# Performance work log

Hardware: AMD Instinct MI355X
Metric: run time of the kernel (lower is better)

Reference implementation:

```python
import jax, jax.numpy as jnp
import numpy as np

IN_F, OUT_F, RANK = 4096, 4096, 64
ALPHA = 128.0
SCALING = ALPHA / RANK  # 2.0
BATCH_TOKENS = 8192


def setup_inputs() -> dict:
    key = jax.random.key(0)
    k1, k2, k3, k4 = jax.random.split(key, 4)
    x = jax.random.normal(k1, (BATCH_TOKENS, IN_F), dtype=jnp.float32)
    weight = jax.random.normal(k2, (OUT_F, IN_F), dtype=jnp.float32) * 0.02
    P = jax.random.normal(k3, (OUT_F, RANK), dtype=jnp.float32) * 0.01
    Lambda = jnp.ones((RANK,), dtype=jnp.float32) * 0.01
    Q = jax.random.normal(k4, (RANK, IN_F), dtype=jnp.float32) * 0.01
    rank_mask = jnp.ones((RANK,), dtype=jnp.bool_)
    return {"x": x, "weight": weight, "P": P, "Lambda": Lambda, "Q": Q, "rank_mask": rank_mask}


def reference(x, weight, P, Lambda, Q, rank_mask):
    # active_Lambda = Lambda * mask; delta_W = (P * active_Lambda) @ Q  -> [OUT_F, IN_F]
    active_Lambda = Lambda * rank_mask.astype(Lambda.dtype)
    delta_W = (P * active_Lambda[None, :]) @ Q
    # F.linear(x, W_eff) = x @ W_eff^T
    W_eff = weight + SCALING * delta_W
    return x @ W_eff.T
```

## Files before the change

kernel.cpp:

```cpp
#include <hip/hip_runtime.h>
#include <hip/hip_bf16.h>
#include <stdint.h>

#define M_TOK 8192
#define NF    4096
#define KF    4096
#define RANK  64

typedef __attribute__((ext_vector_type(8))) short short8;
typedef __attribute__((ext_vector_type(4))) float floatx4;

typedef const uint32_t __attribute__((address_space(1)))* gp1_t;
typedef uint32_t __attribute__((address_space(3)))* lp3_t;

__device__ __forceinline__ void load_lds16(const void* g, void* l) {
  __builtin_amdgcn_global_load_lds((gp1_t)g, (lp3_t)l, 16, 0, 0);
}

__global__ void cast_f32_bf16(const float* __restrict__ in,
                              __hip_bfloat16* __restrict__ out) {
  size_t i = ((size_t)blockIdx.x * blockDim.x + threadIdx.x) * 8;
  float4 a = *(const float4*)(in + i);
  float4 b = *(const float4*)(in + i + 4);
  union { __hip_bfloat16 h[8]; uint4 u; } pk;
  pk.h[0] = __float2bfloat16(a.x);
  pk.h[1] = __float2bfloat16(a.y);
  pk.h[2] = __float2bfloat16(a.z);
  pk.h[3] = __float2bfloat16(a.w);
  pk.h[4] = __float2bfloat16(b.x);
  pk.h[5] = __float2bfloat16(b.y);
  pk.h[6] = __float2bfloat16(b.z);
  pk.h[7] = __float2bfloat16(b.w);
  *(uint4*)(out + i) = pk.u;
}

__global__ __launch_bounds__(256) void build_weff(
    const float* __restrict__ W, const float* __restrict__ P,
    const float* __restrict__ Lam, const float* __restrict__ Q,
    const unsigned char* __restrict__ mask,
    __hip_bfloat16* __restrict__ Wb) {
  __shared__ float lam[RANK];
  __shared__ float plT[RANK][68];
  __shared__ float Qs[RANK][68];

  const int t = threadIdx.x;
  const int n0 = blockIdx.y * 64;
  const int k0 = blockIdx.x * 64;

  if (t < RANK) lam[t] = 2.0f * Lam[t] * (mask[t] ? 1.0f : 0.0f);
  __syncthreads();

  {
    const int nl = t & 63;
    const int rg = (t >> 6) * 16;
    const float* p = P + (size_t)(n0 + nl) * RANK + rg;
#pragma unroll
    for (int j = 0; j < 16; j += 4) {
      float4 v = *(const float4*)(p + j);
      plT[rg + j + 0][nl] = v.x * lam[rg + j + 0];
      plT[rg + j + 1][nl] = v.y * lam[rg + j + 1];
      plT[rg + j + 2][nl] = v.z * lam[rg + j + 2];
      plT[rg + j + 3][nl] = v.w * lam[rg + j + 3];
    }
    const int r = t >> 2;
    const int kc = (t & 3) * 16;
    const float* q = Q + (size_t)r * KF + k0 + kc;
#pragma unroll
    for (int j = 0; j < 16; j += 4) {
      float4 v = *(const float4*)(q + j);
      Qs[r][kc + j + 0] = v.x;
      Qs[r][kc + j + 1] = v.y;
      Qs[r][kc + j + 2] = v.z;
      Qs[r][kc + j + 3] = v.w;
    }
  }
  __syncthreads();

  const int tn4 = t >> 4;
  const int tk4 = t & 15;
  float accv[4][4];
#pragma unroll
  for (int i = 0; i < 4; i++) {
    float4 w = *(const float4*)(W + (size_t)(n0 + tn4 * 4 + i) * KF + k0 + tk4 * 4);
    accv[i][0] = w.x; accv[i][1] = w.y; accv[i][2] = w.z; accv[i][3] = w.w;
  }
#pragma unroll 8
  for (int r = 0; r < RANK; r++) {
    float4 p4 = *(const float4*)&plT[r][tn4 * 4];
    float4 q4 = *(const float4*)&Qs[r][tk4 * 4];
#define ROWFMA(i, pi)                                                  \
    accv[i][0] += (pi) * q4.x; accv[i][1] += (pi) * q4.y;              \
    accv[i][2] += (pi) * q4.z; accv[i][3] += (pi) * q4.w;
    ROWFMA(0, p4.x) ROWFMA(1, p4.y) ROWFMA(2, p4.z) ROWFMA(3, p4.w)
#undef ROWFMA
  }
#pragma unroll
  for (int i = 0; i < 4; i++) {
    union { __hip_bfloat16 h[4]; uint2 u; } pk;
    pk.h[0] = __float2bfloat16(accv[i][0]);
    pk.h[1] = __float2bfloat16(accv[i][1]);
    pk.h[2] = __float2bfloat16(accv[i][2]);
    pk.h[3] = __float2bfloat16(accv[i][3]);
    *(uint2*)(Wb + (size_t)(n0 + tn4 * 4 + i) * KF + k0 + tk4 * 4) = pk.u;
  }
}

#define BM 256
#define BN 256
#define BK 64
#define NT (KF / BK)
#define ASL 16384

#define SB0 __builtin_amdgcn_sched_barrier(0)
#define BARSYNC do { SB0; __builtin_amdgcn_s_barrier(); } while (0)
#define LGK(n) do { asm volatile("s_waitcnt lgkmcnt(" #n ")" ::: "memory"); SB0; } while (0)

__device__ __forceinline__ void read_a4(short8 (&afr)[2][2],
                                        const __hip_bfloat16* Asl,
                                        int row_base, int swz) {
#pragma unroll
  for (int mm = 0; mm < 2; ++mm)
#pragma unroll
    for (int ks = 0; ks < 2; ++ks)
      afr[mm][ks] = *(const short8*)(Asl + ks * 8192 + (row_base + mm * 16) * 32 + swz);
}

__device__ __forceinline__ void read_b8(short8 (&bfr)[4][2],
                                        const __hip_bfloat16* Bsl,
                                        int brow, int swz) {
#pragma unroll
  for (int nf = 0; nf < 4; ++nf)
#pragma unroll
    for (int ks = 0; ks < 2; ++ks)
      bfr[nf][ks] = *(const short8*)(Bsl + ks * 8192 + (brow + nf * 16) * 32 + swz);
}

template <int P>
__device__ __forceinline__ void mfma16(floatx4 (&acc)[8][4],
                                       const short8 (&afr)[2][2],
                                       const short8 (&bfr)[4][2]) {
#pragma unroll
  for (int ks = 0; ks < 2; ++ks)
#pragma unroll
    for (int mm = 0; mm < 2; ++mm)
#pragma unroll
      for (int nf = 0; nf < 4; ++nf)
        acc[P * 2 + mm][nf] = __builtin_amdgcn_mfma_f32_16x16x32_bf16(
            afr[mm][ks], bfr[nf][ks], acc[P * 2 + mm][nf], 0, 0, 0);
}

__global__ __launch_bounds__(512, 2) void gemm_xwt(
    const __hip_bfloat16* __restrict__ A,
    const __hip_bfloat16* __restrict__ B,
    float* __restrict__ C) {
  extern __shared__ __hip_bfloat16 lds[];
  __hip_bfloat16* As = lds;
  __hip_bfloat16* Bs = lds + 2 * ASL;
  const __hip_bfloat16* As0 = As;
  const __hip_bfloat16* As1 = As + ASL;
  const __hip_bfloat16* Bs0 = Bs;
  const __hip_bfloat16* Bs1 = Bs + ASL;

  const int t = threadIdx.x;
  const int lane = t & 63;
  const int wave = t >> 6;
  const int wm = wave >> 2;
  const int wn = wave & 3;
  const int frow = lane & 15;
  const int kq = lane >> 4;
  const int swz = ((kq + (frow >> 1)) & 3) * 8;

  const int bid = blockIdx.x;
  const int wk = (bid & 7) * 64 + (bid >> 3);
  const int bm = wk >> 4;
  const int bn = wk & 15;

  const int c = ((t & 3) - ((t >> 3) & 3)) & 3;
  const __hip_bfloat16* a_src = A + (size_t)(bm * BM + (t >> 2)) * KF + c * 8;
  const __hip_bfloat16* b_src = B + (size_t)(bn * BN + (t >> 2)) * KF + c * 8;
  __hip_bfloat16* a_dst = As + t * 8;
  __hip_bfloat16* b_dst = Bs + t * 8;

#define STAGE_A(kt_, slot_, h_)                                                        \
  do {                                                                                 \
    const __hip_bfloat16* s_ = a_src + ((kt_) & (NT - 1)) * BK + (size_t)(h_) * 128 * KF; \
    __hip_bfloat16* d_ = a_dst + (slot_) * ASL + (h_) * 4096;                          \
    load_lds16(s_, d_);                                                \
    load_lds16(s_ + 32, d_ + 8192);                                    \
  } while (0)
#define STAGE_B(kt_, slot_, h_)                                                        \
  do {                                                                                 \
    const __hip_bfloat16* s_ = b_src + ((kt_) & (NT - 1)) * BK + (size_t)(h_) * 128 * KF; \
    __hip_bfloat16* d_ = b_dst + (slot_) * ASL + (h_) * 4096;                          \
    load_lds16(s_, d_);                                                                \
    load_lds16(s_ + 32, d_ + 8192);                                                    \
  } while (0)

  floatx4 acc[8][4] = {};
  short8 bE[4][2], bO[4][2];
  short8 aX[2][2], aY[2][2];

  const int arow = wm * 128 + frow;
  const int brow = wn * 64 + frow;

  STAGE_A(0, 0, 0); STAGE_A(0, 0, 1);
  STAGE_B(0, 0, 0); STAGE_B(0, 0, 1);
  STAGE_B(1, 1, 0); STAGE_B(1, 1, 1);
  asm volatile("s_waitcnt vmcnt(4)" ::: "memory");
  __builtin_amdgcn_s_barrier();
  read_b8(bE, Bs0, brow, swz);
  read_a4(aX, As0, arow + 0 * 32, swz);

  for (int kt = 0; kt < NT; kt += 2) {
    read_a4(aY, As0, arow + 1 * 32, swz);
    STAGE_A(kt + 1, 1, 0);
    BARSYNC; LGK(4);
    __builtin_amdgcn_s_setprio(1); mfma16<0>(acc, aX, bE); __builtin_amdgcn_s_setprio(0);
    BARSYNC;
    read_a4(aX, As0, arow + 2 * 32, swz);
    STAGE_A(kt + 1, 1, 1);
    BARSYNC; LGK(4);
    __builtin_amdgcn_s_setprio(1); mfma16<1>(acc, aY, bE); __builtin_amdgcn_s_setprio(0);
    BARSYNC;
    read_a4(aY, As0, arow + 3 * 32, swz);
    STAGE_B(kt + 2, 0, 0);
    BARSYNC; LGK(4);
    __builtin_amdgcn_s_setprio(1); mfma16<2>(acc, aX, bE); __builtin_amdgcn_s_setprio(0);
    SB0;
    asm volatile("s_waitcnt vmcnt(2)" ::: "memory");
    __builtin_amdgcn_s_barrier();
    read_b8(bO, Bs1, brow, swz);
    read_a4(aX, As1, arow + 0 * 32, swz);
    STAGE_B(kt + 2, 0, 1);
    BARSYNC; LGK(12);
    __builtin_amdgcn_s_setprio(1); mfma16<3>(acc, aY, bE); __builtin_amdgcn_s_setprio(0);
    BARSYNC;

    read_a4(aY, As1, arow + 1 * 32, swz);
    STAGE_A(kt + 2, 0, 0);
    BARSYNC; LGK(4);
    __builtin_amdgcn_s_setprio(1); mfma16<0>(acc, aX, bO); __builtin_amdgcn_s_setprio(0);
    BARSYNC;
    read_a4(aX, As1, arow + 2 * 32, swz);
    STAGE_A(kt + 2, 0, 1);
    BARSYNC; LGK(4);
    __builtin_amdgcn_s_setprio(1); mfma16<1>(acc, aY, bO); __builtin_amdgcn_s_setprio(0);
    BARSYNC;
    read_a4(aY, As1, arow + 3 * 32, swz);
    STAGE_B(kt + 3, 1, 0);
    BARSYNC; LGK(4);
    __builtin_amdgcn_s_setprio(1); mfma16<2>(acc, aX, bO); __builtin_amdgcn_s_setprio(0);
    SB0;
    asm volatile("s_waitcnt vmcnt(2)" ::: "memory");
    __builtin_amdgcn_s_barrier();
    read_b8(bE, Bs0, brow, swz);
    read_a4(aX, As0, arow + 0 * 32, swz);
    STAGE_B(kt + 3, 1, 1);
    BARSYNC; LGK(12);
    __builtin_amdgcn_s_setprio(1); mfma16<3>(acc, aY, bO); __builtin_amdgcn_s_setprio(0);
    BARSYNC;
  }

#undef STAGE_A
#undef STAGE_B

  const int col0 = bn * BN + wn * 64 + (lane & 15);
  const int row0 = bm * BM + wm * 128 + (lane >> 4) * 4;
#pragma unroll
  for (int mf = 0; mf < 8; ++mf)
#pragma unroll
    for (int nf = 0; nf < 4; ++nf)
#pragma unroll
      for (int r = 0; r < 4; ++r)
        C[(size_t)(row0 + mf * 16 + r) * NF + (col0 + nf * 16)] = acc[mf][nf][r];
}

extern "C" void kernel_launch(void* const* d_in, const int* in_sizes, int n_in,
                              void* d_out, int out_size, void* d_ws, size_t ws_size,
                              hipStream_t stream) {
  const float* x      = (const float*)d_in[0];
  const float* weight = (const float*)d_in[1];
  const float* P      = (const float*)d_in[2];
  const float* Lam    = (const float*)d_in[3];
  const float* Q      = (const float*)d_in[4];
  const unsigned char* mask = (const unsigned char*)d_in[5];
  float* out = (float*)d_out;

  __hip_bfloat16* Xb = (__hip_bfloat16*)d_ws;
  __hip_bfloat16* Wb = (__hip_bfloat16*)((char*)d_ws + (size_t)M_TOK * KF * 2);

  static int smem_set = 0;
  if (!smem_set) {
    hipFuncSetAttribute((const void*)gemm_xwt,
                        hipFuncAttributeMaxDynamicSharedMemorySize, 131072);
    smem_set = 1;
  }

  cast_f32_bf16<<<(M_TOK * KF) / (256 * 8), 256, 0, stream>>>(x, Xb);
  build_weff<<<dim3(KF / 64, NF / 64), 256, 0, stream>>>(weight, P, Lam, Q, mask, Wb);
  gemm_xwt<<<dim3((M_TOK / BM) * (NF / BN)), 512, 131072, stream>>>(Xb, Wb, out);
}
```

Baseline: 531.8 us.

## Merge prep kernels into one launch and restructure GEMM A/B prefetch schedule

Combines the x-to-bf16 cast and the W_eff build into a single prep kernel that branches on block index, removing one kernel launch and the gap between the two. In the GEMM main loop, the A and B global-to-LDS staging is reordered: A for the next two k-tiles is prefetched up front, B stages are issued early in each half-iteration, and A stages move after the LDS reads, with vmcnt thresholds raised to match. The aim is to keep more loads in flight and hide memory latency better. The new ordering relies on hand-tuned waitcnt values, so any mismatch could cause races or extra stalls.

```diff
diff --git a/kernel.cpp b/kernel.cpp
--- a/kernel.cpp
+++ b/kernel.cpp
@@ -17,35 +17,35 @@
   __builtin_amdgcn_global_load_lds((gp1_t)g, (lp3_t)l, 16, 0, 0);
 }
 
-__global__ void cast_f32_bf16(const float* __restrict__ in,
-                              __hip_bfloat16* __restrict__ out) {
-  size_t i = ((size_t)blockIdx.x * blockDim.x + threadIdx.x) * 8;
-  float4 a = *(const float4*)(in + i);
-  float4 b = *(const float4*)(in + i + 4);
-  union { __hip_bfloat16 h[8]; uint4 u; } pk;
-  pk.h[0] = __float2bfloat16(a.x);
-  pk.h[1] = __float2bfloat16(a.y);
-  pk.h[2] = __float2bfloat16(a.z);
-  pk.h[3] = __float2bfloat16(a.w);
-  pk.h[4] = __float2bfloat16(b.x);
-  pk.h[5] = __float2bfloat16(b.y);
-  pk.h[6] = __float2bfloat16(b.z);
-  pk.h[7] = __float2bfloat16(b.w);
-  *(uint4*)(out + i) = pk.u;
-}
-
-__global__ __launch_bounds__(256) void build_weff(
-    const float* __restrict__ W, const float* __restrict__ P,
-    const float* __restrict__ Lam, const float* __restrict__ Q,
-    const unsigned char* __restrict__ mask,
-    __hip_bfloat16* __restrict__ Wb) {
+#define CASTX_BLOCKS ((M_TOK * KF) / (256 * 8))
+__global__ __launch_bounds__(256) void prep_all(
+    const float* __restrict__ x, const float* __restrict__ W,
+    const float* __restrict__ P, const float* __restrict__ Lam,
+    const float* __restrict__ Q, const unsigned char* __restrict__ mask,
+    __hip_bfloat16* __restrict__ Xb, __hip_bfloat16* __restrict__ Wb) {
   __shared__ float lam[RANK];
   __shared__ float plT[RANK][68];
   __shared__ float Qs[RANK][68];
 
+  const int bid = blockIdx.x;
   const int t = threadIdx.x;
-  const int n0 = blockIdx.y * 64;
-  const int k0 = blockIdx.x * 64;
+
+  if (bid < CASTX_BLOCKS) {
+    size_t i = ((size_t)bid * 256 + t) * 8;
+    float4 a = *(const float4*)(x + i);
+    float4 b = *(const float4*)(x + i + 4);
+    union { __hip_bfloat16 h[8]; uint4 u; } pk;
+    pk.h[0] = __float2bfloat16(a.x); pk.h[1] = __float2bfloat16(a.y);
+    pk.h[2] = __float2bfloat16(a.z); pk.h[3] = __float2bfloat16(a.w);
+    pk.h[4] = __float2bfloat16(b.x); pk.h[5] = __float2bfloat16(b.y);
+    pk.h[6] = __float2bfloat16(b.z); pk.h[7] = __float2bfloat16(b.w);
+    *(uint4*)(Xb + i) = pk.u;
+    return;
+  }
+
+  const int idx = bid - CASTX_BLOCKS;
+  const int n0 = (idx >> 6) * 64;
+  const int k0 = (idx & 63) * 64;
 
   if (t < RANK) lam[t] = 2.0f * Lam[t] * (mask[t] ? 1.0f : 0.0f);
   __syncthreads();
@@ -205,58 +205,61 @@
 
   STAGE_A(0, 0, 0); STAGE_A(0, 0, 1);
   STAGE_B(0, 0, 0); STAGE_B(0, 0, 1);
+  STAGE_A(1, 1, 0); STAGE_A(1, 1, 1);
   STAGE_B(1, 1, 0); STAGE_B(1, 1, 1);
-  asm volatile("s_waitcnt vmcnt(4)" ::: "memory");
+  asm volatile("s_waitcnt vmcnt(8)" ::: "memory");
   __builtin_amdgcn_s_barrier();
   read_b8(bE, Bs0, brow, swz);
   read_a4(aX, As0, arow + 0 * 32, swz);
 
   for (int kt = 0; kt < NT; kt += 2) {
     read_a4(aY, As0, arow + 1 * 32, swz);
-    STAGE_A(kt + 1, 1, 0);
+    STAGE_B(kt + 2, 0, 0);
     BARSYNC; LGK(4);
     __builtin_amdgcn_s_setprio(1); mfma16<0>(acc, aX, bE); __builtin_amdgcn_s_setprio(0);
     BARSYNC;
     read_a4(aX, As0, arow + 2 * 32, swz);
-    STAGE_A(kt + 1, 1, 1);
+    STAGE_B(kt + 2, 0, 1);
     BARSYNC; LGK(4);
     __builtin_amdgcn_s_setprio(1); mfma16<1>(acc, aY, bE); __builtin_amdgcn_s_setprio(0);
     BARSYNC;
     read_a4(aY, As0, arow + 3 * 32, swz);
-    STAGE_B(kt + 2, 0, 0);
     BARSYNC; LGK(4);
     __builtin_amdgcn_s_setprio(1); mfma16<2>(acc, aX, bE); __builtin_amdgcn_s_setprio(0);
     SB0;
-    asm volatile("s_waitcnt vmcnt(2)" ::: "memory");
+    asm volatile("s_waitcnt vmcnt(4)" ::: "memory");
     __builtin_amdgcn_s_barrier();
     read_b8(bO, Bs1, brow, swz);
     read_a4(aX, As1, arow + 0 * 32, swz);
-    STAGE_B(kt + 2, 0, 1);
     BARSYNC; LGK(12);
+    STAGE_A(kt + 2, 0, 0);
+    STAGE_A(kt + 2, 0, 1);
+    SB0;
     __builtin_amdgcn_s_setprio(1); mfma16<3>(acc, aY, bE); __builtin_amdgcn_s_setprio(0);
     BARSYNC;
 
     read_a4(aY, As1, arow + 1 * 32, swz);
-    STAGE_A(kt + 2, 0, 0);
+    STAGE_B(kt + 3, 1, 0);
     BARSYNC; LGK(4);
     __builtin_amdgcn_s_setprio(1); mfma16<0>(acc, aX, bO); __builtin_amdgcn_s_setprio(0);
     BARSYNC;
     read_a4(aX, As1, arow + 2 * 32, swz);
-    STAGE_A(kt + 2, 0, 1);
+    STAGE_B(kt + 3, 1, 1);
     BARSYNC; LGK(4);
     __builtin_amdgcn_s_setprio(1); mfma16<1>(acc, aY, bO); __builtin_amdgcn_s_setprio(0);
     BARSYNC;
     read_a4(aY, As1, arow + 3 * 32, swz);
-    STAGE_B(kt + 3, 1, 0);
     BARSYNC; LGK(4);
     __builtin_amdgcn_s_setprio(1); mfma16<2>(acc, aX, bO); __builtin_amdgcn_s_setprio(0);
     SB0;
-    asm volatile("s_waitcnt vmcnt(2)" ::: "memory");
+    asm volatile("s_waitcnt vmcnt(4)" ::: "memory");
     __builtin_amdgcn_s_barrier();
     read_b8(bE, Bs0, brow, swz);
     read_a4(aX, As0, arow + 0 * 32, swz);
-    STAGE_B(kt + 3, 1, 1);
     BARSYNC; LGK(12);
+    STAGE_A(kt + 3, 1, 0);
+    STAGE_A(kt + 3, 1, 1);
+    SB0;
     __builtin_amdgcn_s_setprio(1); mfma16<3>(acc, aY, bO); __builtin_amdgcn_s_setprio(0);
     BARSYNC;
   }
@@ -296,7 +299,7 @@
     smem_set = 1;
   }
 
-  cast_f32_bf16<<<(M_TOK * KF) / (256 * 8), 256, 0, stream>>>(x, Xb);
-  build_weff<<<dim3(KF / 64, NF / 64), 256, 0, stream>>>(weight, P, Lam, Q, mask, Wb);
+  prep_all<<<CASTX_BLOCKS + (NF / 64) * (KF / 64), 256, 0, stream>>>(
+      x, weight, P, Lam, Q, mask, Xb, Wb);
   gemm_xwt<<<dim3((M_TOK / BM) * (NF / BN)), 512, 131072, stream>>>(Xb, Wb, out);
 }
```

Result: faster. 517.0 us (-2.8%).
